# Kernel tuning notes

Hardware: AMD Instinct MI355X
Metric: run time of the kernel (lower is better)

## Reference

```python
import jax, jax.numpy as jnp
import numpy as np

N_ELEC = 8192   # electrons (nodes)
N_NUC = 512     # nuclei
EMB = 256       # embedding_dim
KER = 256       # kernel_dim
DF = 64         # dist_feat_dim
MID = 128       # round(sqrt(DF*KER)), log-interpolated hidden width of w-MLP
E = 131072      # edges per edge type


def _ssp(x):
    # shifted softplus, deepqmc default activation: log(0.5*exp(x) + 0.5)
    return jax.nn.softplus(x) - jnp.log(2.0)


def setup_inputs() -> dict:
    key = jax.random.key(0)
    ks = jax.random.split(key, 24)
    def nrm(k, shape, scale):
        return jax.random.normal(k, shape, dtype=jnp.float32) * scale
    inp = {}
    inp['electrons'] = nrm(ks[0], (N_ELEC, EMB), 1.0)
    inp['nuclei'] = nrm(ks[1], (N_NUC, KER), 1.0)
    for i, lbl in enumerate(['same', 'anti', 'n']):
        inp[f'dist_{lbl}'] = jax.random.uniform(ks[2 + i], (E, DF), dtype=jnp.float32)
        inp[f'w1_{lbl}'] = nrm(ks[5 + i], (DF, MID), DF ** -0.5)
        inp[f'b1_{lbl}'] = jnp.zeros((MID,), jnp.float32)
        inp[f'w2_{lbl}'] = nrm(ks[8 + i], (MID, KER), MID ** -0.5)
        inp[f'g_{lbl}'] = nrm(ks[11 + i], (KER, EMB), KER ** -0.5)
    inp['h_w'] = nrm(ks[14], (EMB, KER), EMB ** -0.5)
    inp['senders_same'] = jax.random.randint(ks[15], (E,), 0, N_ELEC)
    inp['senders_anti'] = jax.random.randint(ks[16], (E,), 0, N_ELEC)
    inp['senders_n'] = jax.random.randint(ks[17], (E,), 0, N_NUC)
    inp['receivers_same'] = jax.random.randint(ks[18], (E,), 0, N_ELEC)
    inp['receivers_anti'] = jax.random.randint(ks[19], (E,), 0, N_ELEC)
    inp['receivers_n'] = jax.random.randint(ks[20], (E,), 0, N_ELEC)
    return inp


def reference(electrons, nuclei, dist_same, dist_anti, dist_n,
              w1_same, b1_same, w2_same, w1_anti, b1_anti, w2_anti,
              w1_n, b1_n, w2_n, g_same, g_anti, g_n, h_w,
              senders_same, senders_anti, senders_n,
              receivers_same, receivers_anti, receivers_n):
    def w_mlp(d, w1, b1, w2):
        # MLP with ('log', 2) hidden layers: linear+bias -> SSP -> last linear (no bias)
        return _ssp(d @ w1 + b1) @ w2

    # per-edge filters from distance features: [E, KER]
    we_same = w_mlp(dist_same, w1_same, b1_same, w2_same)
    we_anti = w_mlp(dist_anti, w1_anti, b1_anti, w2_anti)
    we_n = w_mlp(dist_n, w1_n, b1_n, w2_n)

    # shared h (single bias-free linear) on gathered sender electrons: [E, KER]
    hx_same = electrons[senders_same] @ h_w
    hx_anti = electrons[senders_anti] @ h_w

    weh_same = we_same * hx_same
    weh_anti = we_anti * hx_anti
    weh_n = we_n * nuclei[senders_n]

    # scatter-sum messages to receiver electrons: [N_ELEC, KER]
    z_same = jax.ops.segment_sum(weh_same, receivers_same, num_segments=N_ELEC)
    z_anti = jax.ops.segment_sum(weh_anti, receivers_anti, num_segments=N_ELEC)
    z_n = jax.ops.segment_sum(weh_n, receivers_n, num_segments=N_ELEC)

    # per-label g (single bias-free linear) + residual update, order matches original
    return electrons + (z_n @ g_n + z_same @ g_same + z_anti @ g_anti)
```

## Files before the change

### kernel.cpp

```cpp
#include <hip/hip_runtime.h>
#include <stdint.h>


#define N_ELEC 8192
#define N_NUC  512
#define EMB    256
#define KER    256
#define DF     64
#define MID    128
#define NEDGE  131072
#define RPS    8256
#define CSTR   272
#define NSLOT  16

using u16 = unsigned short;
using u64 = unsigned long long;
typedef short short8 __attribute__((ext_vector_type(8)));
typedef float f32x4 __attribute__((ext_vector_type(4)));

__device__ __forceinline__ float bf2f(u16 h) {
  return __uint_as_float(((unsigned)h) << 16);
}
__device__ __forceinline__ u16 f2bf(float f) {
  unsigned u = __float_as_uint(f);
  return (u16)((u + 0x7FFFu + ((u >> 16) & 1u)) >> 16);
}
__device__ __forceinline__ unsigned pkbf(float a, float b) {
  return ((unsigned)f2bf(b) << 16) | (unsigned)f2bf(a);
}
__device__ __forceinline__ float ssp_fast(float x) {
  const float e = __expf(-fabsf(x));
  return fmaxf(x, 0.f) + __logf(fmaf(0.5f, e, 0.5f));
}

__device__ __forceinline__ void bar_lds() {
  __builtin_amdgcn_sched_barrier(0);
  asm volatile("s_waitcnt lgkmcnt(0)" ::: "memory");
  __builtin_amdgcn_s_barrier();
  __builtin_amdgcn_sched_barrier(0);
}

__device__ __forceinline__ void stage_t64(const char* g0, long stride,
                                          char* lds, int tid) {
  const int l = tid & 63, w = tid >> 6;
  const int r = w * 16 + (l >> 2);
  const int cb = (l & 3) * 16;
  __builtin_amdgcn_global_load_lds(
      (const __attribute__((address_space(1))) unsigned*)(g0 +
                                                          (long)r * stride +
                                                          cb),
      (__attribute__((address_space(3))) unsigned*)(lds + w * 1024), 16, 0, 0);
}
__device__ __forceinline__ void stage_f64(const float* g0, int stride_e,
                                          int kt, char* lds, int tid) {
#pragma unroll
  for (int k = 0; k < 4; ++k) {
    const int idx2 = k * 256 + tid;
    const int row = idx2 >> 4, cp = idx2 & 15;
    const float2 v = *(const float2*)(g0 + (long)row * stride_e + kt + cp * 2);
    *(unsigned*)(lds + row * 64 + cp * 4) = pkbf(v.x, v.y);
  }
}
template <bool A_F32>
__device__ __forceinline__ void gemm64(const char* A0, long as_bytes,
                                       const float* Af, int as_elems,
                                       const char* B0, long bs, int K,
                                       char* As, char* Bs, f32x4 acc[2][2],
                                       int tid) {
  const int l = tid & 63, lane15 = l & 15, quad = l >> 4, wv = tid >> 6;
  const int mw = (wv >> 1) * 32, nw = (wv & 1) * 32;
  for (int kt = 0; kt < K; kt += 32) {
    if (A_F32)
      stage_f64(Af, as_elems, kt, As, tid);
    else
      stage_t64(A0 + (long)kt * 2, as_bytes, As, tid);
    stage_t64(B0 + (long)kt * 2, bs, Bs, tid);
    __syncthreads();
    short8 af[2], bf[2];
#pragma unroll
    for (int i = 0; i < 2; ++i) {
      af[i] = *(const short8*)(As + (mw + i * 16 + lane15) * 64 + quad * 16);
      bf[i] = *(const short8*)(Bs + (nw + i * 16 + lane15) * 64 + quad * 16);
    }
#pragma unroll
    for (int mi = 0; mi < 2; ++mi)
#pragma unroll
      for (int ni = 0; ni < 2; ++ni)
        acc[mi][ni] = __builtin_amdgcn_mfma_f32_16x16x32_bf16(
            af[mi], bf[ni], acc[mi][ni], 0, 0, 0);
    __syncthreads();
  }
}

__global__ __launch_bounds__(256) void k_setup(
    const float* h_w, const float* w1s, const float* w1a, const float* w1n,
    const float* w2s, const float* w2a, const float* w2n, const float* gs,
    const float* ga, const float* gn, u16* hwT, u16* w1T, u16* w2T, u16* gT,
    float4* z, int* cnt) {
  const int b = blockIdx.x;
  if (b < 6144) {
    z[b * 256 + threadIdx.x] = (float4){0.f, 0.f, 0.f, 0.f};
    return;
  }
  if (b < 6240) {
    cnt[(b - 6144) * 256 + threadIdx.x] = 0;
    return;
  }
  int i = (b - 6240) * 256 + threadIdx.x;
  if (i < 65536) {
    int n = i >> 8, k = i & 255;
    hwT[i] = f2bf(h_w[k * 256 + n]);
    return;
  }
  int j = i - 65536;
  if (j < 24576) {
    int t = j >> 13, jj = j & 8191, n = jj >> 6, k = jj & 63;
    const float* w1 = t == 0 ? w1s : (t == 1 ? w1a : w1n);
    w1T[j] = f2bf(w1[k * 128 + n]);
    return;
  }
  j -= 24576;
  if (j < 98304) {
    int t = j >> 15, jj = j & 32767, n = jj >> 7, k = jj & 127;
    const float* w2 = t == 0 ? w2s : (t == 1 ? w2a : w2n);
    w2T[j] = f2bf(w2[k * 256 + n]);
    return;
  }
  j -= 98304;
  if (j < 196608) {
    int n = j / 768, q = j % 768, t = q >> 8, k = q & 255;
    const float* g = t == 0 ? gs : (t == 1 ? ga : gn);
    gT[j] = f2bf(g[k * 256 + n]);
  }
}

__global__ __launch_bounds__(256) void k_hist(const int* r0, const int* r1,
                                              const int* r2, int* cnt) {
  const int t = blockIdx.z;
  const int* rcv = t == 0 ? r0 : (t == 1 ? r1 : r2);
  const int e = blockIdx.x * 256 + threadIdx.x;
  atomicAdd(&cnt[t * N_ELEC + rcv[e]], 1);
}

__global__ __launch_bounds__(256) void k_scan(const int* cnt, int* rowptr,
                                              int* cursor) {
  const int t = blockIdx.x, tid = threadIdx.x;
  __shared__ int part[256];
  const int* c = cnt + t * N_ELEC;
  int s = 0;
#pragma unroll
  for (int i = 0; i < 32; ++i) s += c[tid * 32 + i];
  part[tid] = s;
  __syncthreads();
  for (int off = 1; off < 256; off <<= 1) {
    int v = (tid >= off) ? part[tid - off] : 0;
    __syncthreads();
    part[tid] += v;
    __syncthreads();
  }
  int run = (tid == 0) ? 0 : part[tid - 1];
  int* rp = rowptr + t * RPS;
  int* cu = cursor + t * N_ELEC;
  for (int i = 0; i < 32; ++i) {
    rp[tid * 32 + i] = run;
    cu[tid * 32 + i] = run;
    run += c[tid * 32 + i];
  }
  if (tid == 255) rp[N_ELEC] = run;
}

__global__ __launch_bounds__(256) void k_place(const int* r0, const int* r1,
                                               const int* r2, const int* s0,
                                               const int* s1, const int* s2,
                                               int* cursor, u64* pk) {
  const int t = blockIdx.z;
  const int* rcv = t == 0 ? r0 : (t == 1 ? r1 : r2);
  const int* snd = t == 0 ? s0 : (t == 1 ? s1 : s2);
  const int e = blockIdx.x * 256 + threadIdx.x;
  const int rr = rcv[e];
  const int pos = atomicAdd(&cursor[t * N_ELEC + rr], 1);
  pk[t * NEDGE + pos] =
      (u64)(unsigned)e | ((u64)(unsigned)snd[e] << 17) | ((u64)(unsigned)rr << 30);
}

__global__ __launch_bounds__(256) void k_he(const float* elec, const u16* hwT,
                                            u16* he) {
  __shared__ char As[4096], Bs[4096];
  f32x4 acc[2][2];
#pragma unroll
  for (int i = 0; i < 2; ++i)
#pragma unroll
    for (int j = 0; j < 2; ++j) acc[i][j] = (f32x4){0.f, 0.f, 0.f, 0.f};
  const int m0 = blockIdx.x * 64, n0 = blockIdx.y * 64;
  gemm64<true>(nullptr, 0, elec + (long)m0 * 256, 256,
               (const char*)hwT + (long)n0 * 512, 512, 256, As, Bs, acc,
               threadIdx.x);
  const int l = threadIdx.x & 63, lane15 = l & 15, quad = l >> 4,
            wv = threadIdx.x >> 6;
  const int mw = (wv >> 1) * 32, nw = (wv & 1) * 32;
#pragma unroll
  for (int mi = 0; mi < 2; ++mi)
#pragma unroll
    for (int r = 0; r < 4; ++r) {
      const int row = m0 + mw + mi * 16 + quad * 4 + r;
#pragma unroll
      for (int ni = 0; ni < 2; ++ni) {
        const int col = n0 + nw + ni * 16 + lane15;
        he[row * 256 + col] = f2bf(acc[mi][ni][r]);
      }
    }
}

__global__ __launch_bounds__(256, 3) void k_edge(
    const float* d0, const float* d1, const float* d2, const float* b0,
    const float* b1p, const float* b2, const u16* w1T, const u16* w2T,
    const u16* he, const float* nucf, const u64* pk, float* z) {
  __shared__ char mid[128 * CSTR];
  __shared__ char hc[32 * CSTR];
  __shared__ float zacc[NSLOT][128];
  __shared__ int snd_l[128], rcv_l[128], slot_l[128];
  __shared__ int rcv_slot[NSLOT];
  __shared__ int cnt_w[2], nslots_s;

  const int t = blockIdx.z;
  const int m0 = blockIdx.x * 128;
  const int tid = threadIdx.x;
  const float* dist = t == 0 ? d0 : (t == 1 ? d1 : d2);
  const float* bias = t == 0 ? b0 : (t == 1 ? b1p : b2);
  const u16* w1t = w1T + t * 8192;
  const u16* w2t = w2T + t * 32768;
  const bool is_nuc = (t == 2);
  const u64* pkt = pk + (size_t)t * NEDGE + m0;

  if (tid < 128) {
    const u64 rec = pkt[tid];
    snd_l[tid] = (int)((rec >> 17) & 0x1FFFu);
    rcv_l[tid] = (int)(rec >> 30);
  }
  {
    float* zf = &zacc[0][0];
#pragma unroll
    for (int i = 0; i < 8; ++i) zf[i * 256 + tid] = 0.f;
  }
  int rows[4];
#pragma unroll
  for (int s = 0; s < 4; ++s)
    rows[s] = (int)(pkt[(s * 256 + tid) >> 3] & 0x1FFFFu);
#pragma unroll
  for (int j = 0; j < 2; ++j)
#pragma unroll
    for (int s = 0; s < 4; ++s) {
      const int idx = s * 256 + tid, row = idx >> 3, ch = idx & 7;
      const float4 v =
          *(const float4*)(dist + (long)rows[s] * 64 + j * 32 + ch * 4);
      uint2 p;
      p.x = pkbf(v.x, v.y);
      p.y = pkbf(v.z, v.w);
      *(uint2*)(mid + j * 8192 + row * 64 + ch * 8) = p;
    }
  bar_lds();

  {
    bool flag = false;
    int pre = 0;
    if (tid < 128) {
      const int rcv = rcv_l[tid];
      flag = (tid > 0) && (rcv != rcv_l[tid - 1]);
      const u64 m = __ballot(flag);
      pre = (int)__popcll(m & ((1ull << (tid & 63)) - 1ull));
      if ((tid & 63) == 0) cnt_w[tid >> 6] = (int)__popcll(m);
    }
    bar_lds();
    if (tid < 128) {
      const int slot = pre + (flag ? 1 : 0) + ((tid >= 64) ? cnt_w[0] : 0);
      slot_l[tid] = slot;
      if ((flag || tid == 0) && slot < NSLOT) rcv_slot[slot] = rcv_l[tid];
      if (tid == 0) nslots_s = cnt_w[0] + cnt_w[1] + 1;
    }
  }

  const int l = tid & 63, lane15 = l & 15, quad = l >> 4, wv = tid >> 6;
  const int mw = (wv >> 1) * 64, nw = (wv & 1) * 64;

  f32x4 acc[4][4];
#pragma unroll
  for (int i = 0; i < 4; ++i)
#pragma unroll
    for (int j = 0; j < 4; ++j) acc[i][j] = (f32x4){0.f, 0.f, 0.f, 0.f};
#pragma unroll
  for (int j = 0; j < 2; ++j) {
    short8 af[4], bf[4];
#pragma unroll
    for (int i = 0; i < 4; ++i) {
      af[i] = *(const short8*)(mid + j * 8192 + (mw + i * 16 + lane15) * 64 +
                               quad * 16);
      bf[i] = *(const short8*)(w1t + (nw + i * 16 + lane15) * 64 + j * 32 +
                               quad * 8);
    }
#pragma unroll
    for (int mi = 0; mi < 4; ++mi)
#pragma unroll
      for (int ni = 0; ni < 4; ++ni)
        acc[mi][ni] = __builtin_amdgcn_mfma_f32_16x16x32_bf16(
            af[mi], bf[ni], acc[mi][ni], 0, 0, 0);
  }
  bar_lds();

#pragma unroll
  for (int mi = 0; mi < 4; ++mi)
#pragma unroll
    for (int r = 0; r < 4; ++r) {
      const int row = mw + mi * 16 + quad * 4 + r;
#pragma unroll
      for (int ni = 0; ni < 4; ++ni) {
        const int col = nw + ni * 16 + lane15;
        const float x = acc[mi][ni][r] + bias[col];
        *(u16*)(mid + row * CSTR + col * 2) = f2bf(ssp_fast(x));
      }
    }
  bar_lds();

  for (int n0 = 0; n0 < 256; n0 += 128) {
#pragma unroll
    for (int i = 0; i < 4; ++i)
#pragma unroll
      for (int j = 0; j < 4; ++j) acc[i][j] = (f32x4){0.f, 0.f, 0.f, 0.f};
#pragma unroll
    for (int kt = 0; kt < 128; kt += 32) {
      short8 af[4], bf[4];
#pragma unroll
      for (int i = 0; i < 4; ++i) {
        af[i] = *(const short8*)(mid + (mw + i * 16 + lane15) * CSTR + kt * 2 +
                                 quad * 16);
        bf[i] = *(const short8*)(w2t + (n0 + nw + i * 16 + lane15) * 128 + kt +
                                 quad * 8);
      }
#pragma unroll
      for (int mi = 0; mi < 4; ++mi)
#pragma unroll
        for (int ni = 0; ni < 4; ++ni)
          acc[mi][ni] = __builtin_amdgcn_mfma_f32_16x16x32_bf16(
              af[mi], bf[ni], acc[mi][ni], 0, 0, 0);
    }

#pragma unroll
    for (int q = 0; q < 4; ++q) {
      const int rbase = q * 32;
      if (!is_nuc) {
#pragma unroll
        for (int c = 0; c < 2; ++c) {
          const int chunk = c * 256 + tid;
          const int row = chunk >> 4, off = chunk & 15;
          const uint4 v =
              *(const uint4*)((const char*)he +
                              (size_t)snd_l[rbase + row] * 512 + n0 * 2 +
                              off * 16);
          *(uint4*)(hc + row * CSTR + off * 16) = v;
        }
      } else {
#pragma unroll
        for (int c = 0; c < 2; ++c) {
          const int chunk = c * 256 + tid;
          const int row = chunk >> 4, off = chunk & 15;
          const char* src = (const char*)nucf +
                            (size_t)snd_l[rbase + row] * 1024 + n0 * 4 +
                            off * 32;
          const float4 a = *(const float4*)src;
          const float4 b = *(const float4*)(src + 16);
          uint4 p;
          p.x = pkbf(a.x, a.y);
          p.y = pkbf(a.z, a.w);
          p.z = pkbf(b.x, b.y);
          p.w = pkbf(b.z, b.w);
          *(uint4*)(hc + row * CSTR + off * 16) = p;
        }
      }
      bar_lds();

      if ((wv >> 1) == (q >> 1)) {
        const int mi0 = (q & 1) * 2;
#pragma unroll
        for (int mi2 = 0; mi2 < 2; ++mi2) {
          const int mi = mi0 + mi2;
#pragma unroll
          for (int r = 0; r < 4; ++r) {
            const int lrow = mi2 * 16 + quad * 4 + r;
#pragma unroll
            for (int ni = 0; ni < 4; ++ni) {
              const int col = nw + ni * 16 + lane15;
              u16* p = (u16*)(hc + lrow * CSTR) + col;
              *p = f2bf(acc[mi][ni][r] * bf2f(*p));
            }
          }
        }
      }
      bar_lds();

      {
        const int cp = l;
        const int lr0 = wv * 8;
        float a0 = 0.f, a1 = 0.f;
        int cs = slot_l[rbase + lr0];
#pragma unroll
        for (int i = 0; i < 8; ++i) {
          const int lr = lr0 + i, gr = rbase + lr;
          const unsigned p = *(const unsigned*)(hc + lr * CSTR + cp * 4);
          a0 += __uint_as_float(p << 16);
          a1 += __uint_as_float(p & 0xffff0000u);
          const int ns = (i + 1 < 8) ? slot_l[gr + 1] : -1;
          if (ns != cs) {
            if (cs < NSLOT) {
              atomicAdd(&zacc[cs][cp * 2], a0);
              atomicAdd(&zacc[cs][cp * 2 + 1], a1);
            } else {
              float* zp =
                  z + (size_t)rcv_l[gr] * 768 + t * 256 + n0 + cp * 2;
              unsafeAtomicAdd(zp, a0);
              unsafeAtomicAdd(zp + 1, a1);
            }
            a0 = a1 = 0.f;
            cs = ns;
          }
        }
      }
      bar_lds();
    }

    {
      const int nsl = nslots_s;
      const int s = tid >> 4, c0 = (tid & 15) * 8;
      if (s < nsl && s < NSLOT) {
        const int r = rcv_slot[s];
        float* zp = z + (size_t)r * 768 + t * 256 + n0 + c0;
        if (s == 0 || s == nsl - 1) {
#pragma unroll
          for (int jj = 0; jj < 8; ++jj)
            unsafeAtomicAdd(zp + jj, zacc[s][c0 + jj]);
        } else {
          *(float4*)zp = *(float4*)&zacc[s][c0];
          *(float4*)(zp + 4) = *(float4*)&zacc[s][c0 + 4];
        }
      }
    }
    bar_lds();
    {
      float* zf = &zacc[0][0];
#pragma unroll
      for (int i = 0; i < 8; ++i) zf[i * 256 + tid] = 0.f;
    }
  }
}

__global__ __launch_bounds__(256) void k_final(const float* z, const u16* gT,
                                               const float* elec, float* out) {
  __shared__ char As[4096], Bs[4096];
  f32x4 acc[2][2];
#pragma unroll
  for (int i = 0; i < 2; ++i)
#pragma unroll
    for (int j = 0; j < 2; ++j) acc[i][j] = (f32x4){0.f, 0.f, 0.f, 0.f};
  const int m0 = blockIdx.x * 64, n0 = blockIdx.y * 64;
  gemm64<true>(nullptr, 0, z + (long)m0 * 768, 768,
               (const char*)gT + (long)n0 * 1536, 1536, 768, As, Bs, acc,
               threadIdx.x);
  const int l = threadIdx.x & 63, lane15 = l & 15, quad = l >> 4,
            wv = threadIdx.x >> 6;
  const int mw = (wv >> 1) * 32, nw = (wv & 1) * 32;
#pragma unroll
  for (int mi = 0; mi < 2; ++mi)
#pragma unroll
    for (int r = 0; r < 4; ++r) {
      const int row = m0 + mw + mi * 16 + quad * 4 + r;
#pragma unroll
      for (int ni = 0; ni < 2; ++ni) {
        const int col = n0 + nw + ni * 16 + lane15;
        out[row * 256 + col] = acc[mi][ni][r] + elec[row * 256 + col];
      }
    }
}

extern "C" void kernel_launch(void* const* d_in, const int* in_sizes, int n_in,
                              void* d_out, int out_size, void* d_ws,
                              size_t ws_size, hipStream_t stream) {
  int I_dist[3], I_w1[3], I_b1[3], I_w2[3], I_g[3], I_hw;
  if (in_sizes[3] == 64 * 128) {
    for (int t = 0; t < 3; ++t) {
      I_dist[t] = 2 + t * 5 + 0;
      I_w1[t] = 2 + t * 5 + 1;
      I_b1[t] = 2 + t * 5 + 2;
      I_w2[t] = 2 + t * 5 + 3;
      I_g[t] = 2 + t * 5 + 4;
    }
    I_hw = 17;
  } else {
    I_dist[0] = 2; I_dist[1] = 3; I_dist[2] = 4;
    I_w1[0] = 5;  I_b1[0] = 6;  I_w2[0] = 7;
    I_w1[1] = 8;  I_b1[1] = 9;  I_w2[1] = 10;
    I_w1[2] = 11; I_b1[2] = 12; I_w2[2] = 13;
    I_g[0] = 14; I_g[1] = 15; I_g[2] = 16;
    I_hw = 17;
  }
  const int I_snd[3] = {18, 19, 20};
  const int I_rcv[3] = {21, 22, 23};

  char* ws = (char*)d_ws;
  u16* he = (u16*)(ws + 0);
  u16* hwT = (u16*)(ws + 4194304);
  u16* w1T = (u16*)(ws + 4325376);
  u16* w2T = (u16*)(ws + 4374528);
  u16* gT = (u16*)(ws + 4571136);
  float* z = (float*)(ws + 4964352);
  int* cnt = (int*)(ws + 30130176);
  int* rowptr = (int*)(ws + 30228480);
  int* cursor = (int*)(ws + 30327552);
  u64* pk = (u64*)(ws + 30425856);

  const float* elec = (const float*)d_in[0];
  const float* nuc = (const float*)d_in[1];
  const int* s0 = (const int*)d_in[I_snd[0]];
  const int* s1 = (const int*)d_in[I_snd[1]];
  const int* s2 = (const int*)d_in[I_snd[2]];
  const int* r0 = (const int*)d_in[I_rcv[0]];
  const int* r1 = (const int*)d_in[I_rcv[1]];
  const int* r2 = (const int*)d_in[I_rcv[2]];

  k_setup<<<7744, 256, 0, stream>>>(
      (const float*)d_in[I_hw], (const float*)d_in[I_w1[0]],
      (const float*)d_in[I_w1[1]], (const float*)d_in[I_w1[2]],
      (const float*)d_in[I_w2[0]], (const float*)d_in[I_w2[1]],
      (const float*)d_in[I_w2[2]], (const float*)d_in[I_g[0]],
      (const float*)d_in[I_g[1]], (const float*)d_in[I_g[2]], hwT, w1T, w2T,
      gT, (float4*)z, cnt);

  k_hist<<<dim3(NEDGE / 256, 1, 3), 256, 0, stream>>>(r0, r1, r2, cnt);
  k_scan<<<3, 256, 0, stream>>>(cnt, rowptr, cursor);
  k_place<<<dim3(NEDGE / 256, 1, 3), 256, 0, stream>>>(r0, r1, r2, s0, s1, s2,
                                                       cursor, pk);

  k_he<<<dim3(N_ELEC / 64, 4), 256, 0, stream>>>(elec, hwT, he);

  k_edge<<<dim3(NEDGE / 128, 1, 3), 256, 0, stream>>>(
      (const float*)d_in[I_dist[0]], (const float*)d_in[I_dist[1]],
      (const float*)d_in[I_dist[2]], (const float*)d_in[I_b1[0]],
      (const float*)d_in[I_b1[1]], (const float*)d_in[I_b1[2]], w1T, w2T, he,
      nuc, pk, z);

  k_final<<<dim3(N_ELEC / 64, 4), 256, 0, stream>>>(z, gT, elec,
                                                    (float*)d_out);
}
```

Baseline: 453.7 us.

## Use 512-thread blocks in edge kernel and stage all 128 sender rows at once

The edge kernel now runs 8 waves per block instead of 4, with each wave owning a 32x64 output sub-tile, which halves the accumulator registers per thread. The sender-feature staging buffer grows from 32 to 128 rows, so the four-pass gather/multiply/reduce loop with its barriers becomes a single pass per output half. This cuts barrier count and raises per-block parallelism for latency hiding, but the larger LDS footprint (roughly 78KB per block) may limit how many blocks fit on a CU.

```diff
diff --git a/kernel.cpp b/kernel.cpp
--- a/kernel.cpp
+++ b/kernel.cpp
@@ -211,13 +211,13 @@
     }
 }
 
-__global__ __launch_bounds__(256, 3) void k_edge(
+__global__ __launch_bounds__(512, 4) void k_edge(
     const float* d0, const float* d1, const float* d2, const float* b0,
     const float* b1p, const float* b2, const u16* w1T, const u16* w2T,
     const u16* he, const float* nucf, const u64* pk, float* z) {
-  __shared__ char mid[128 * CSTR];
-  __shared__ char hc[32 * CSTR];
-  __shared__ float zacc[NSLOT][128];
+  __shared__ __align__(16) char mid[128 * CSTR];
+  __shared__ __align__(16) char hc[128 * CSTR];
+  __shared__ __align__(16) float zacc[NSLOT][128];
   __shared__ int snd_l[128], rcv_l[128], slot_l[128];
   __shared__ int rcv_slot[NSLOT];
   __shared__ int cnt_w[2], nslots_s;
@@ -240,17 +240,17 @@
   {
     float* zf = &zacc[0][0];
 #pragma unroll
-    for (int i = 0; i < 8; ++i) zf[i * 256 + tid] = 0.f;
-  }
-  int rows[4];
-#pragma unroll
-  for (int s = 0; s < 4; ++s)
-    rows[s] = (int)(pkt[(s * 256 + tid) >> 3] & 0x1FFFFu);
+    for (int i = 0; i < 4; ++i) zf[i * 512 + tid] = 0.f;
+  }
+  int rows[2];
+#pragma unroll
+  for (int s = 0; s < 2; ++s)
+    rows[s] = (int)(pkt[(s * 512 + tid) >> 3] & 0x1FFFFu);
 #pragma unroll
   for (int j = 0; j < 2; ++j)
 #pragma unroll
-    for (int s = 0; s < 4; ++s) {
-      const int idx = s * 256 + tid, row = idx >> 3, ch = idx & 7;
+    for (int s = 0; s < 2; ++s) {
+      const int idx = s * 512 + tid, row = idx >> 3, ch = idx & 7;
       const float4 v =
           *(const float4*)(dist + (long)rows[s] * 64 + j * 32 + ch * 4);
       uint2 p;
@@ -280,25 +280,27 @@
   }
 
   const int l = tid & 63, lane15 = l & 15, quad = l >> 4, wv = tid >> 6;
-  const int mw = (wv >> 1) * 64, nw = (wv & 1) * 64;
-
-  f32x4 acc[4][4];
-#pragma unroll
-  for (int i = 0; i < 4; ++i)
+  const int mw = (wv >> 1) * 32;
+  const int nw = (wv & 1) * 64;
+
+  f32x4 acc[2][4];
+#pragma unroll
+  for (int i = 0; i < 2; ++i)
 #pragma unroll
     for (int j = 0; j < 4; ++j) acc[i][j] = (f32x4){0.f, 0.f, 0.f, 0.f};
 #pragma unroll
   for (int j = 0; j < 2; ++j) {
-    short8 af[4], bf[4];
-#pragma unroll
-    for (int i = 0; i < 4; ++i) {
+    short8 af[2], bf[4];
+#pragma unroll
+    for (int i = 0; i < 2; ++i)
       af[i] = *(const short8*)(mid + j * 8192 + (mw + i * 16 + lane15) * 64 +
                                quad * 16);
+#pragma unroll
+    for (int i = 0; i < 4; ++i)
       bf[i] = *(const short8*)(w1t + (nw + i * 16 + lane15) * 64 + j * 32 +
                                quad * 8);
-    }
-#pragma unroll
-    for (int mi = 0; mi < 4; ++mi)
+#pragma unroll
+    for (int mi = 0; mi < 2; ++mi)
 #pragma unroll
       for (int ni = 0; ni < 4; ++ni)
         acc[mi][ni] = __builtin_amdgcn_mfma_f32_16x16x32_bf16(
@@ -307,7 +309,7 @@
   bar_lds();
 
 #pragma unroll
-  for (int mi = 0; mi < 4; ++mi)
+  for (int mi = 0; mi < 2; ++mi)
 #pragma unroll
     for (int r = 0; r < 4; ++r) {
       const int row = mw + mi * 16 + quad * 4 + r;
@@ -322,131 +324,119 @@
 
   for (int n0 = 0; n0 < 256; n0 += 128) {
 #pragma unroll
-    for (int i = 0; i < 4; ++i)
+    for (int i = 0; i < 2; ++i)
 #pragma unroll
       for (int j = 0; j < 4; ++j) acc[i][j] = (f32x4){0.f, 0.f, 0.f, 0.f};
 #pragma unroll
     for (int kt = 0; kt < 128; kt += 32) {
-      short8 af[4], bf[4];
-#pragma unroll
-      for (int i = 0; i < 4; ++i) {
+      short8 af[2], bf[4];
+#pragma unroll
+      for (int i = 0; i < 2; ++i)
         af[i] = *(const short8*)(mid + (mw + i * 16 + lane15) * CSTR + kt * 2 +
                                  quad * 16);
+#pragma unroll
+      for (int i = 0; i < 4; ++i)
         bf[i] = *(const short8*)(w2t + (n0 + nw + i * 16 + lane15) * 128 + kt +
                                  quad * 8);
-      }
-#pragma unroll
-      for (int mi = 0; mi < 4; ++mi)
+#pragma unroll
+      for (int mi = 0; mi < 2; ++mi)
 #pragma unroll
         for (int ni = 0; ni < 4; ++ni)
           acc[mi][ni] = __builtin_amdgcn_mfma_f32_16x16x32_bf16(
               af[mi], bf[ni], acc[mi][ni], 0, 0, 0);
     }
 
-#pragma unroll
-    for (int q = 0; q < 4; ++q) {
-      const int rbase = q * 32;
-      if (!is_nuc) {
-#pragma unroll
-        for (int c = 0; c < 2; ++c) {
-          const int chunk = c * 256 + tid;
-          const int row = chunk >> 4, off = chunk & 15;
-          const uint4 v =
-              *(const uint4*)((const char*)he +
-                              (size_t)snd_l[rbase + row] * 512 + n0 * 2 +
-                              off * 16);
-          *(uint4*)(hc + row * CSTR + off * 16) = v;
+    if (!is_nuc) {
+#pragma unroll
+      for (int c = 0; c < 4; ++c) {
+        const int chunk = c * 512 + tid;
+        const int row = chunk >> 4, off = chunk & 15;
+        const uint4 v =
+            *(const uint4*)((const char*)he + (size_t)snd_l[row] * 512 +
+                            n0 * 2 + off * 16);
+        *(uint4*)(hc + row * CSTR + off * 16) = v;
+      }
+    } else {
+#pragma unroll
+      for (int c = 0; c < 4; ++c) {
+        const int chunk = c * 512 + tid;
+        const int row = chunk >> 4, off = chunk & 15;
+        const char* src = (const char*)nucf + (size_t)snd_l[row] * 1024 +
+                          n0 * 4 + off * 32;
+        const float4 a = *(const float4*)src;
+        const float4 b = *(const float4*)(src + 16);
+        uint4 p;
+        p.x = pkbf(a.x, a.y);
+        p.y = pkbf(a.z, a.w);
+        p.z = pkbf(b.x, b.y);
+        p.w = pkbf(b.z, b.w);
+        *(uint4*)(hc + row * CSTR + off * 16) = p;
+      }
+    }
+    bar_lds();
+
+#pragma unroll
+    for (int mi = 0; mi < 2; ++mi)
+#pragma unroll
+      for (int r = 0; r < 4; ++r) {
+        const int row = mw + mi * 16 + quad * 4 + r;
+#pragma unroll
+        for (int ni = 0; ni < 4; ++ni) {
+          const int col = nw + ni * 16 + lane15;
+          u16* p = (u16*)(hc + row * CSTR) + col;
+          *p = f2bf(acc[mi][ni][r] * bf2f(*p));
         }
-      } else {
-#pragma unroll
-        for (int c = 0; c < 2; ++c) {
-          const int chunk = c * 256 + tid;
-          const int row = chunk >> 4, off = chunk & 15;
-          const char* src = (const char*)nucf +
-                            (size_t)snd_l[rbase + row] * 1024 + n0 * 4 +
-                            off * 32;
-          const float4 a = *(const float4*)src;
-          const float4 b = *(const float4*)(src + 16);
-          uint4 p;
-          p.x = pkbf(a.x, a.y);
-          p.y = pkbf(a.z, a.w);
-          p.z = pkbf(b.x, b.y);
-          p.w = pkbf(b.z, b.w);
-          *(uint4*)(hc + row * CSTR + off * 16) = p;
+      }
+    bar_lds();
+
+    {
+      const int cp = l;
+      const int rbeg = wv * 16;
+      float a0 = 0.f, a1 = 0.f;
+      int cs = slot_l[rbeg];
+#pragma unroll
+      for (int i = 0; i < 16; ++i) {
+        const int row = rbeg + i;
+        const unsigned p = *(const unsigned*)(hc + row * CSTR + cp * 4);
+        a0 += __uint_as_float(p << 16);
+        a1 += __uint_as_float(p & 0xffff0000u);
+        const int ns = (i + 1 < 16) ? slot_l[row + 1] : -1;
+        if (ns != cs) {
+          if (cs < NSLOT) {
+            atomicAdd(&zacc[cs][cp * 2], a0);
+            atomicAdd(&zacc[cs][cp * 2 + 1], a1);
+          } else {
+            float* zp = z + (size_t)rcv_l[row] * 768 + t * 256 + n0 + cp * 2;
+            unsafeAtomicAdd(zp, a0);
+            unsafeAtomicAdd(zp + 1, a1);
+          }
+          a0 = a1 = 0.f;
+          cs = ns;
         }
       }
-      bar_lds();
-
-      if ((wv >> 1) == (q >> 1)) {
-        const int mi0 = (q & 1) * 2;
-#pragma unroll
-        for (int mi2 = 0; mi2 < 2; ++mi2) {
-          const int mi = mi0 + mi2;
-#pragma unroll
-          for (int r = 0; r < 4; ++r) {
-            const int lrow = mi2 * 16 + quad * 4 + r;
-#pragma unroll
-            for (int ni = 0; ni < 4; ++ni) {
-              const int col = nw + ni * 16 + lane15;
-              u16* p = (u16*)(hc + lrow * CSTR) + col;
-              *p = f2bf(acc[mi][ni][r] * bf2f(*p));
-            }
-          }
-        }
-      }
-      bar_lds();
-
-      {
-        const int cp = l;
-        const int lr0 = wv * 8;
-        float a0 = 0.f, a1 = 0.f;
-        int cs = slot_l[rbase + lr0];
-#pragma unroll
-        for (int i = 0; i < 8; ++i) {
-          const int lr = lr0 + i, gr = rbase + lr;
-          const unsigned p = *(const unsigned*)(hc + lr * CSTR + cp * 4);
-          a0 += __uint_as_float(p << 16);
-          a1 += __uint_as_float(p & 0xffff0000u);
-          const int ns = (i + 1 < 8) ? slot_l[gr + 1] : -1;
-          if (ns != cs) {
-            if (cs < NSLOT) {
-              atomicAdd(&zacc[cs][cp * 2], a0);
-              atomicAdd(&zacc[cs][cp * 2 + 1], a1);
-            } else {
-              float* zp =
-                  z + (size_t)rcv_l[gr] * 768 + t * 256 + n0 + cp * 2;
-              unsafeAtomicAdd(zp, a0);
-              unsafeAtomicAdd(zp + 1, a1);
-            }
-            a0 = a1 = 0.f;
-            cs = ns;
-          }
-        }
-      }
-      bar_lds();
-    }
+    }
+    bar_lds();
 
     {
       const int nsl = nslots_s;
-      const int s = tid >> 4, c0 = (tid & 15) * 8;
+      const int s = tid >> 5, c0 = (tid & 31) * 4;
       if (s < nsl && s < NSLOT) {
         const int r = rcv_slot[s];
         float* zp = z + (size_t)r * 768 + t * 256 + n0 + c0;
         if (s == 0 || s == nsl - 1) {
 #pragma unroll
-          for (int jj = 0; jj < 8; ++jj)
+          for (int jj = 0; jj < 4; ++jj)
             unsafeAtomicAdd(zp + jj, zacc[s][c0 + jj]);
         } else {
           *(float4*)zp = *(float4*)&zacc[s][c0];
-          *(float4*)(zp + 4) = *(float4*)&zacc[s][c0 + 4];
         }
       }
     }
-    bar_lds();
-    {
+    if (n0 == 0) {
+      bar_lds();
       float* zf = &zacc[0][0];
 #pragma unroll
-      for (int i = 0; i < 8; ++i) zf[i * 256 + tid] = 0.f;
+      for (int i = 0; i < 4; ++i) zf[i * 512 + tid] = 0.f;
     }
   }
 }
@@ -539,7 +529,7 @@
 
   k_he<<<dim3(N_ELEC / 64, 4), 256, 0, stream>>>(elec, hwT, he);
 
-  k_edge<<<dim3(NEDGE / 128, 1, 3), 256, 0, stream>>>(
+  k_edge<<<dim3(NEDGE / 128, 1, 3), 512, 0, stream>>>(
       (const float*)d_in[I_dist[0]], (const float*)d_in[I_dist[1]],
       (const float*)d_in[I_dist[2]], (const float*)d_in[I_b1[0]],
       (const float*)d_in[I_b1[1]], (const float*)d_in[I_b1[2]], w1T, w2T, he,
```

Measured after the change: 465.4 us. 2.6% more time.
